# Performance work log

Hardware: AMD Instinct MI355X
Metric: run time of the kernel (lower is better)

Reference implementation:

```python
import jax, jax.numpy as jnp
import numpy as np

GEO_VOCAB = 32          # len(geo_code_char); class dim = GEO_VOCAB + 1 (padding idx)
A_VALUE = 0.8
SEQ = 12                # targets length, fixed by linspace(0,11,12) weight


def _integral(b, num_points=2000):
    # torch.linspace(0, b, 2000) includes endpoints; dx = b / num_points
    x = np.linspace(0.0, b, num_points)
    dx = b / num_points
    return np.sum(np.power(A_VALUE, x) * dx)

# continuous_rewards[0] = padding (0.0); rewards[i+1] = 1/integral(0, i+1)
CONT_REWARDS = np.array([0.0] + [1.0 / _integral(i + 1) for i in range(GEO_VOCAB)],
                        dtype=np.float32)
CORRECT_W = np.power(A_VALUE, np.arange(SEQ, dtype=np.float32)).astype(np.float32)
ERROR_W = (CORRECT_W + 1.0).astype(np.float32)


def _ce_none(logits, targets, ignore_index):
    # logits [B,S,V], targets [B,S]; per-element CE, 0 at ignored positions
    logp = jax.nn.log_softmax(logits, axis=-1)
    tgt = jnp.clip(targets, 0, logits.shape[-1] - 1)
    ce = -jnp.take_along_axis(logp, tgt[..., None], axis=-1)[..., 0]
    return jnp.where(targets == ignore_index, 0.0, ce)


def setup_inputs() -> dict:
    key = jax.random.key(0)
    k1, k2, k3, k4, k5, k6 = jax.random.split(key, 6)
    B, S, V = 131072, 13, GEO_VOCAB + 1
    return {
        "geo_output": jax.random.normal(k1, (B, S - 1, V), dtype=jnp.float32),
        "mask_geo_output": jax.random.normal(k2, (B, S, V), dtype=jnp.float32),
        "pos_geo_code": jax.random.randint(k3, (B, S), 0, V),
        "mask_ground_truth": jax.random.randint(k4, (B, S), 0, V),
        "aux_loss": jax.random.uniform(k5, (), dtype=jnp.float32),
        "token_aux_loss": jax.random.uniform(k6, (), dtype=jnp.float32),
        "sigma": jnp.ones((4,), dtype=jnp.float32),
    }


def reference(geo_output, mask_geo_output, pos_geo_code, mask_ground_truth,
              aux_loss, token_aux_loss, sigma):
    V = geo_output.shape[-1]
    ignore = V - 1  # len(geo_code_char)

    # mask loss: CE with ignore_index=-100, mean over valid positions
    logp_m = jax.nn.log_softmax(mask_geo_output, axis=-1)
    tgt_m = jnp.clip(mask_ground_truth, 0, V - 1)
    ce_m = -jnp.take_along_axis(logp_m, tgt_m[..., None], axis=-1)[..., 0]
    valid = (mask_ground_truth != -100).astype(ce_m.dtype)
    mask_loss = jnp.sum(ce_m * valid) / jnp.maximum(jnp.sum(valid), 1.0)

    # geo CE (reduction='none', ignore_index = V-1)
    targets = pos_geo_code[:, 1:]                       # [B, 12]
    cross_loss = _ce_none(geo_output, targets, ignore)  # [B, 12]

    correct = jnp.argmax(geo_output, axis=-1) == targets  # [B, 12] bool
    correct_mask = correct.astype(cross_loss.dtype)
    error_mask = 1.0 - correct_mask

    # first index where correct==False (argmin of int mask; 0 if all correct)
    min_idx = jnp.argmin(correct.astype(jnp.int32), axis=1)       # [B]
    prefix_mask = (jnp.arange(targets.shape[1]) < min_idx[:, None]).astype(cross_loss.dtype)
    cont = jnp.asarray(CONT_REWARDS)[min_idx][:, None]            # [B, 1]

    prefix_loss = jnp.mean(cross_loss * prefix_mask * cont)
    correct_loss = jnp.mean(cross_loss * correct_mask * jnp.asarray(CORRECT_W))
    error_loss = jnp.mean(cross_loss * error_mask * jnp.asarray(ERROR_W))
    geo_loss = prefix_loss + correct_loss + error_loss

    losses = jnp.stack([geo_loss, mask_loss, aux_loss, token_aux_loss])
    weighted = jnp.sum(0.5 * losses / sigma ** 2) + jnp.log(jnp.prod(sigma))

    return jnp.stack([weighted, prefix_loss, correct_loss, error_loss, mask_loss])
```

## Files before the change

### kernel.cpp

```cpp
#include <hip/hip_runtime.h>
#include <cmath>

#define THREADS 256
#define MTASKS  144
#define GROWS   12
#define SLOTS   64

struct Tables { float cont[13]; float cw[12]; float ew[12]; };

static Tables make_tables() {
    Tables tb;
    tb.cont[0] = 0.0f;
    for (int j = 1; j <= 12; j++) {
        double b = (double)j;
        double s = 0.0;
        for (int k = 0; k < 2000; k++) {
            double x = b * (double)k / 1999.0;
            s += pow(0.8, x);
        }
        double integ = s * (b / 2000.0);
        tb.cont[j] = (float)(1.0 / integ);
    }
    for (int s = 0; s < 12; s++) {
        double w = pow(0.8, (double)s);
        tb.cw[s] = (float)w;
        tb.ew[s] = (float)(w + 1.0);
    }
    return tb;
}

__global__ void zero_acc(double* g) {
    int t = threadIdx.x;
    if (t < 5 * SLOTS) g[t] = 0.0;
}

__global__ __launch_bounds__(THREADS, 8) void loss_fused(
    const float* __restrict__ geo,
    const float* __restrict__ mgo,
    const int*   __restrict__ pos,
    const int*   __restrict__ mgt,
    double*      __restrict__ gacc,
    int B, int geoBlocks, Tables tb)
{
    __shared__ float buf[4752];
    __shared__ float s_ce[GROWS * 12];
    __shared__ int   s_corr[GROWS * 12];
    __shared__ float sh_cont[13];
    __shared__ float sh_cw[12];
    __shared__ float sh_ew[12];
    __shared__ float red[4][3];

    const int t = threadIdx.x;
    float v0 = 0.0f, v1 = 0.0f, v2 = 0.0f;
    const bool isGeo = (blockIdx.x < (unsigned)geoBlocks);

    if (isGeo) {
        const long long row0 = (long long)blockIdx.x * GROWS;
        const int nrows = min(GROWS, (int)(B - row0));
        const int ntask = nrows * 12;
        const int r = t / 12, s = t - (t / 12) * 12;
        int tg = 0;
        if (t < ntask) tg = pos[(row0 + r) * 13 + s + 1];
        if (t == 0) {
            #pragma unroll
            for (int j = 0; j < 13; j++) sh_cont[j] = tb.cont[j];
            #pragma unroll
            for (int j = 0; j < 12; j++) { sh_cw[j] = tb.cw[j]; sh_ew[j] = tb.ew[j]; }
        }
        {
            const float4* src4 = reinterpret_cast<const float4*>(geo + row0 * 396);
            float4* dst4 = reinterpret_cast<float4*>(buf);
            const int nf4 = nrows * 99;
            for (int i = t; i < nf4; i += THREADS) dst4[i] = src4[i];
        }
        __syncthreads();

        if (t < ntask) {
            const float* x = buf + r * 396 + s * 33;
            float xv[33];
            #pragma unroll
            for (int k = 0; k < 33; k++) xv[k] = x[k];
            float m = xv[0]; int am = 0;
            #pragma unroll
            for (int k = 1; k < 33; k++) { if (xv[k] > m) { m = xv[k]; am = k; } }
            float sum = 0.0f;
            #pragma unroll
            for (int k = 0; k < 33; k++) sum += __expf(xv[k] - m);
            float lse = __logf(sum) + m;
            int tc = tg < 0 ? 0 : (tg > 32 ? 32 : tg);
            float xtc = 0.0f;
            #pragma unroll
            for (int k = 0; k < 33; k++) { if (k == tc) xtc = xv[k]; }
            float ce = (tg == 32) ? 0.0f : (lse - xtc);
            bool corr = (am == tg);
            v1 = corr ? ce * sh_cw[s] : 0.0f;
            v2 = corr ? 0.0f : ce * sh_ew[s];
            s_ce[t] = ce;
            s_corr[t] = corr ? 1 : 0;
        }
        __syncthreads();

        if (t < nrows) {
            float ps = 0.0f; int mi = 12;
            for (int s2 = 0; s2 < 12; s2++) {
                if (!s_corr[t * 12 + s2]) { mi = s2; break; }
                ps += s_ce[t * 12 + s2];
            }
            v0 = (mi >= 12) ? 0.0f : ps * sh_cont[mi];
        }
    } else {
        const long long totalTasks = (long long)B * 13;
        const long long base = (long long)(blockIdx.x - geoBlocks) * MTASKS;
        const int cnt = (int)min((long long)MTASKS, totalTasks - base);
        int tg = 0;
        if (t < cnt) tg = mgt[base + t];
        {
            const float* src = mgo + base * 33;
            const int nf = cnt * 33, nf4 = nf >> 2;
            const float4* src4 = reinterpret_cast<const float4*>(src);
            float4* dst4 = reinterpret_cast<float4*>(buf);
            for (int i = t; i < nf4; i += THREADS) dst4[i] = src4[i];
            for (int i = (nf4 << 2) + t; i < nf; i += THREADS) buf[i] = src[i];
        }
        __syncthreads();

        if (t < cnt) {
            const float* x = buf + t * 33;
            float xv[33];
            #pragma unroll
            for (int k = 0; k < 33; k++) xv[k] = x[k];
            float m = xv[0];
            #pragma unroll
            for (int k = 1; k < 33; k++) m = fmaxf(m, xv[k]);
            float sum = 0.0f;
            #pragma unroll
            for (int k = 0; k < 33; k++) sum += __expf(xv[k] - m);
            float lse = __logf(sum) + m;
            int tc = tg < 0 ? 0 : (tg > 32 ? 32 : tg);
            float xtc = 0.0f;
            #pragma unroll
            for (int k = 0; k < 33; k++) { if (k == tc) xtc = xv[k]; }
            if (tg != -100) { v0 = lse - xtc; v1 = 1.0f; }
        }
    }

    #pragma unroll
    for (int off = 32; off; off >>= 1) {
        v0 += __shfl_down(v0, off, 64);
        v1 += __shfl_down(v1, off, 64);
        v2 += __shfl_down(v2, off, 64);
    }
    const int wid = t >> 6, lane = t & 63;
    if (lane == 0) { red[wid][0] = v0; red[wid][1] = v1; red[wid][2] = v2; }
    __syncthreads();
    if (t == 0) {
        float a0 = 0, a1 = 0, a2 = 0;
        for (int w = 0; w < 4; w++) { a0 += red[w][0]; a1 += red[w][1]; a2 += red[w][2]; }
        const int slot = blockIdx.x & (SLOTS - 1);
        if (isGeo) {
            atomicAdd(&gacc[2 * SLOTS + slot], (double)a0);
            atomicAdd(&gacc[3 * SLOTS + slot], (double)a1);
            atomicAdd(&gacc[4 * SLOTS + slot], (double)a2);
        } else {
            atomicAdd(&gacc[0 * SLOTS + slot], (double)a0);
            atomicAdd(&gacc[1 * SLOTS + slot], (double)a1);
        }
    }
}

__global__ void finalize(const double* __restrict__ g,
                         const float* __restrict__ aux,
                         const float* __restrict__ taux,
                         const float* __restrict__ sigma,
                         float* __restrict__ out, double denom)
{
    const int i = threadIdx.x;
    double a[5];
    #pragma unroll
    for (int q = 0; q < 5; q++) a[q] = g[q * SLOTS + i];
    #pragma unroll
    for (int off = 32; off; off >>= 1) {
        #pragma unroll
        for (int q = 0; q < 5; q++) a[q] += __shfl_down(a[q], off, 64);
    }
    if (i == 0) {
        double mask_loss = a[0] / fmax(a[1], 1.0);
        double prefix = a[2] / denom, corrL = a[3] / denom, errL = a[4] / denom;
        double geoL = prefix + corrL + errL;
        double L[4] = { geoL, mask_loss, (double)aux[0], (double)taux[0] };
        double wsum = 0.0, prod = 1.0;
        for (int q = 0; q < 4; q++) {
            double sg = (double)sigma[q];
            wsum += 0.5 * L[q] / (sg * sg);
            prod *= sg;
        }
        wsum += log(prod);
        out[0] = (float)wsum;
        out[1] = (float)prefix;
        out[2] = (float)corrL;
        out[3] = (float)errL;
        out[4] = (float)mask_loss;
    }
}

extern "C" void kernel_launch(void* const* d_in, const int* in_sizes, int n_in,
                              void* d_out, int out_size, void* d_ws, size_t ws_size,
                              hipStream_t stream)
{
    static Tables tb = make_tables();

    const float* geo   = (const float*)d_in[0];
    const float* mgo   = (const float*)d_in[1];
    const int*   pos   = (const int*)d_in[2];
    const int*   mgt   = (const int*)d_in[3];
    const float* aux   = (const float*)d_in[4];
    const float* taux  = (const float*)d_in[5];
    const float* sigma = (const float*)d_in[6];
    float* out = (float*)d_out;

    const int B = in_sizes[2] / 13;
    double* gacc = (double*)d_ws;

    const int geoBlocks  = (B + GROWS - 1) / GROWS;
    const long long maskTasks = (long long)B * 13;
    const int maskBlocks = (int)((maskTasks + MTASKS - 1) / MTASKS);
    const int totalBlocks = geoBlocks + maskBlocks;

    hipLaunchKernelGGL(zero_acc, dim3(1), dim3(512), 0, stream, gacc);
    hipLaunchKernelGGL(loss_fused, dim3(totalBlocks), dim3(THREADS), 0, stream,
                       geo, mgo, pos, mgt, gacc, B, geoBlocks, tb);
    hipLaunchKernelGGL(finalize, dim3(1), dim3(64), 0, stream,
                       gacc, aux, taux, sigma, out, (double)B * 12.0);
}
```

Before: 446.8 us.

## Stage logits with direct global-to-LDS loads and enlarge per-block tasks

Replaces the register-staged float4 copy into shared memory with __builtin_amdgcn_global_load_lds DMA-style loads, so the data skips VGPRs on its way to LDS. Raises rows per geo block to 16 and mask tasks per block to 192, and lowers the launch_bounds occupancy hint from 8 to 5. Rewrites the max and exp-sum reductions as four independent chains, reads the target logit with an indexed LDS load, and derives argmax-correctness by comparing that logit to the max. The correctness test can differ from first-index argmax when values tie, and the larger LDS footprint per block reduces occupancy.

```diff
diff --git a/kernel.cpp b/kernel.cpp
--- a/kernel.cpp
+++ b/kernel.cpp
@@ -2,8 +2,9 @@
 #include <cmath>
 
 #define THREADS 256
-#define MTASKS  144
-#define GROWS   12
+#define TASKS   192
+#define GROWS   16
+#define MTASKS  192
 #define SLOTS   64
 
 struct Tables { float cont[13]; float cw[12]; float ew[12]; };
@@ -34,7 +35,13 @@
     if (t < 5 * SLOTS) g[t] = 0.0;
 }
 
-__global__ __launch_bounds__(THREADS, 8) void loss_fused(
+typedef __attribute__((address_space(3))) unsigned int* LdsPtr;
+typedef const __attribute__((address_space(1))) unsigned int* GblPtr;
+__device__ __forceinline__ LdsPtr to_lds(const void* p) {
+    return (LdsPtr)(unsigned int)(unsigned long long)p;
+}
+
+__global__ __launch_bounds__(THREADS, 5) void loss_fused(
     const float* __restrict__ geo,
     const float* __restrict__ mgo,
     const int*   __restrict__ pos,
@@ -42,15 +49,16 @@
     double*      __restrict__ gacc,
     int B, int geoBlocks, Tables tb)
 {
-    __shared__ float buf[4752];
-    __shared__ float s_ce[GROWS * 12];
-    __shared__ int   s_corr[GROWS * 12];
+    __shared__ float buf[TASKS * 33];
+    __shared__ float s_ce[TASKS];
+    __shared__ int   s_corr[TASKS];
     __shared__ float sh_cont[13];
     __shared__ float sh_cw[12];
     __shared__ float sh_ew[12];
     __shared__ float red[4][3];
 
     const int t = threadIdx.x;
+    const int wid = t >> 6, lane = t & 63;
     float v0 = 0.0f, v1 = 0.0f, v2 = 0.0f;
     const bool isGeo = (blockIdx.x < (unsigned)geoBlocks);
 
@@ -68,35 +76,46 @@
             for (int j = 0; j < 12; j++) { sh_cw[j] = tb.cw[j]; sh_ew[j] = tb.ew[j]; }
         }
         {
-            const float4* src4 = reinterpret_cast<const float4*>(geo + row0 * 396);
-            float4* dst4 = reinterpret_cast<float4*>(buf);
-            const int nf4 = nrows * 99;
-            for (int i = t; i < nf4; i += THREADS) dst4[i] = src4[i];
+            const float* src = geo + row0 * 396;
+            const int nf16 = nrows * 99;
+            for (int c = wid * 64; c < nf16; c += 256) {
+                const int idx = c + lane;
+                if (idx < nf16)
+                    __builtin_amdgcn_global_load_lds((GblPtr)(src + idx * 4),
+                                                     to_lds(buf + c * 4), 16, 0, 0);
+            }
         }
         __syncthreads();
 
         if (t < ntask) {
-            const float* x = buf + r * 396 + s * 33;
+            const int base = t * 33;
             float xv[33];
             #pragma unroll
-            for (int k = 0; k < 33; k++) xv[k] = x[k];
-            float m = xv[0]; int am = 0;
-            #pragma unroll
-            for (int k = 1; k < 33; k++) { if (xv[k] > m) { m = xv[k]; am = k; } }
-            float sum = 0.0f;
-            #pragma unroll
-            for (int k = 0; k < 33; k++) sum += __expf(xv[k] - m);
-            float lse = __logf(sum) + m;
-            int tc = tg < 0 ? 0 : (tg > 32 ? 32 : tg);
-            float xtc = 0.0f;
-            #pragma unroll
-            for (int k = 0; k < 33; k++) { if (k == tc) xtc = xv[k]; }
-            float ce = (tg == 32) ? 0.0f : (lse - xtc);
-            bool corr = (am == tg);
+            for (int k = 0; k < 33; k++) xv[k] = buf[base + k];
+            float m0 = fmaxf(xv[0], xv[1]), m1 = fmaxf(xv[2], xv[3]);
+            float m2 = fmaxf(xv[4], xv[5]), m3 = fmaxf(xv[6], xv[7]);
+            #pragma unroll
+            for (int k = 8; k < 32; k += 4) {
+                m0 = fmaxf(m0, xv[k]);     m1 = fmaxf(m1, xv[k + 1]);
+                m2 = fmaxf(m2, xv[k + 2]); m3 = fmaxf(m3, xv[k + 3]);
+            }
+            const float m = fmaxf(fmaxf(fmaxf(m0, m1), fmaxf(m2, m3)), xv[32]);
+            float p0 = 0, p1 = 0, p2 = 0, p3 = 0;
+            #pragma unroll
+            for (int k = 0; k < 32; k += 4) {
+                p0 += __expf(xv[k] - m);     p1 += __expf(xv[k + 1] - m);
+                p2 += __expf(xv[k + 2] - m); p3 += __expf(xv[k + 3] - m);
+            }
+            const float sum = (p0 + p1) + (p2 + p3) + __expf(xv[32] - m);
+            const float lse = __logf(sum) + m;
+            const int tc = tg < 0 ? 0 : (tg > 32 ? 32 : tg);
+            const float xtc = buf[base + tc];
+            const float ce = (tg == 32) ? 0.0f : (lse - xtc);
+            const int corr = (tg == tc && xtc == m) ? 1 : 0;
             v1 = corr ? ce * sh_cw[s] : 0.0f;
             v2 = corr ? 0.0f : ce * sh_ew[s];
             s_ce[t] = ce;
-            s_corr[t] = corr ? 1 : 0;
+            s_corr[t] = corr;
         }
         __syncthreads();
 
@@ -116,30 +135,41 @@
         if (t < cnt) tg = mgt[base + t];
         {
             const float* src = mgo + base * 33;
-            const int nf = cnt * 33, nf4 = nf >> 2;
-            const float4* src4 = reinterpret_cast<const float4*>(src);
-            float4* dst4 = reinterpret_cast<float4*>(buf);
-            for (int i = t; i < nf4; i += THREADS) dst4[i] = src4[i];
-            for (int i = (nf4 << 2) + t; i < nf; i += THREADS) buf[i] = src[i];
+            const int nfl = cnt * 33;
+            const int nf16 = nfl >> 2;
+            for (int c = wid * 64; c < nf16; c += 256) {
+                const int idx = c + lane;
+                if (idx < nf16)
+                    __builtin_amdgcn_global_load_lds((GblPtr)(src + idx * 4),
+                                                     to_lds(buf + c * 4), 16, 0, 0);
+            }
+            for (int i = (nf16 << 2) + t; i < nfl; i += THREADS) buf[i] = src[i];
         }
         __syncthreads();
 
         if (t < cnt) {
-            const float* x = buf + t * 33;
+            const int base2 = t * 33;
             float xv[33];
             #pragma unroll
-            for (int k = 0; k < 33; k++) xv[k] = x[k];
-            float m = xv[0];
-            #pragma unroll
-            for (int k = 1; k < 33; k++) m = fmaxf(m, xv[k]);
-            float sum = 0.0f;
-            #pragma unroll
-            for (int k = 0; k < 33; k++) sum += __expf(xv[k] - m);
-            float lse = __logf(sum) + m;
-            int tc = tg < 0 ? 0 : (tg > 32 ? 32 : tg);
-            float xtc = 0.0f;
-            #pragma unroll
-            for (int k = 0; k < 33; k++) { if (k == tc) xtc = xv[k]; }
+            for (int k = 0; k < 33; k++) xv[k] = buf[base2 + k];
+            float m0 = fmaxf(xv[0], xv[1]), m1 = fmaxf(xv[2], xv[3]);
+            float m2 = fmaxf(xv[4], xv[5]), m3 = fmaxf(xv[6], xv[7]);
+            #pragma unroll
+            for (int k = 8; k < 32; k += 4) {
+                m0 = fmaxf(m0, xv[k]);     m1 = fmaxf(m1, xv[k + 1]);
+                m2 = fmaxf(m2, xv[k + 2]); m3 = fmaxf(m3, xv[k + 3]);
+            }
+            const float m = fmaxf(fmaxf(fmaxf(m0, m1), fmaxf(m2, m3)), xv[32]);
+            float p0 = 0, p1 = 0, p2 = 0, p3 = 0;
+            #pragma unroll
+            for (int k = 0; k < 32; k += 4) {
+                p0 += __expf(xv[k] - m);     p1 += __expf(xv[k + 1] - m);
+                p2 += __expf(xv[k + 2] - m); p3 += __expf(xv[k + 3] - m);
+            }
+            const float sum = (p0 + p1) + (p2 + p3) + __expf(xv[32] - m);
+            const float lse = __logf(sum) + m;
+            const int tc = tg < 0 ? 0 : (tg > 32 ? 32 : tg);
+            const float xtc = buf[base2 + tc];
             if (tg != -100) { v0 = lse - xtc; v1 = 1.0f; }
         }
     }
@@ -150,7 +180,6 @@
         v1 += __shfl_down(v1, off, 64);
         v2 += __shfl_down(v2, off, 64);
     }
-    const int wid = t >> 6, lane = t & 63;
     if (lane == 0) { red[wid][0] = v0; red[wid][1] = v1; red[wid][2] = v2; }
     __syncthreads();
     if (t == 0) {
```

Result: no change. 441.3 us (-1.2%).
